# Kernel tuning notes

Hardware: AMD Instinct MI355X
Metric: run time of the kernel (lower is better)

## Reference

```python
import jax, jax.numpy as jnp
import numpy as np

DT = 0.01
NLAG = 50           # int(maxlag / dt), maxlag = 0.5 s
NMA = 20
NC = 8192
NT = 4096


def _xcorr(data1, data2):
    # torch F.conv1d(data1.view(1, nc, nt), data2.view(nc, 1, nt),
    #                padding=NLAG+1, groups=nc)
    # == per-channel sliding cross-correlation.
    lhs = data1[None]            # (1, NC, NT)
    rhs = data2[:, None, :]      # (NC, 1, NT) -- one tiny filter per group
    out = jax.lax.conv_general_dilated(
        lhs, rhs,
        window_strides=(1,),
        padding=[(NLAG + 1, NLAG + 1)],
        dimension_numbers=("NCH", "OIH", "NCH"),
        feature_group_count=NC,
    )
    return out                   # (1, NC, L), L = 2*NLAG + 3 when nt1 == nt2


def _moving_average(x, nma=NMA):
    # Faithful to CCModel.moving_average: AvgPool1d(nma, stride=1, pad=nma//2)
    # applied after permute(0,2,1), i.e. the pooling runs over the CHANNEL
    # axis, with zero padding included in the mean (count_include_pad=True),
    # then sliced back to nc channels.
    nb, nc, L = x.shape
    pad = nma // 2
    xp = jnp.pad(x, ((0, 0), (pad, pad), (0, 0)))
    cs = jnp.concatenate(
        [jnp.zeros((nb, 1, L), x.dtype), jnp.cumsum(xp, axis=1)], axis=1)
    win = (cs[:, nma:, :] - cs[:, :-nma, :]) / nma   # sliding sum / nma
    return win[:, :nc, :]


def _pick_maxabs(R, dt):
    # pick_Rkt_maxabs: per-channel max-|cc| pick.
    L = R.shape[-1]
    nlag_c = (L - 1) // 2        # zero-lag index
    imax = jnp.argmax(jnp.abs(R), axis=-1)                              # (nb, nc)
    vmain = jnp.take_along_axis(R, imax[..., None], axis=-1)[..., 0]    # signed peak
    vpos = jnp.max(R, axis=-1)
    vneg = jnp.min(R, axis=-1)
    vside = jnp.where(vmain >= 0, vneg, vpos)        # opposite-sign extremum
    tmax = (imax - nlag_c).astype(R.dtype) * dt
    return vmain, vside, tmax


def setup_inputs() -> dict:
    key = jax.random.key(0)
    k1, k2, k3, k4 = jax.random.split(key, 4)
    data1 = jax.random.normal(k1, (NC, NT), dtype=jnp.float32)
    data2 = jax.random.normal(k2, (NC, NT), dtype=jnp.float32)
    event1 = jax.random.randint(k3, (1,), 0, 1000, dtype=jnp.int32)
    event2 = jax.random.randint(k4, (1,), 0, 1000, dtype=jnp.int32)
    return {"data1": data1, "data2": data2, "event1": event1, "event2": event2}


def reference(data1, data2, event1, event2):
    xcor = _xcorr(data1, data2)              # (1, NC, 2*NLAG+3)
    xcor = _moving_average(xcor, NMA)        # in-place overwrite in torch
    vmax, vmin, tmax = _pick_maxabs(xcor, DT)
    return xcor, vmax, vmin, tmax
```

## Files before the change

kernel.cpp:

```cpp
#include <hip/hip_runtime.h>

#define NC 8192
#define NT 4096
#define NLAGS 103
#define WS_STRIDE 104
#define LPW 28
#define PADL 51
#define D1LOG 4208
#define PHYS(x) ((x) + (((x) >> 4) << 2))
#define D1P 5260
#define D2P 5120
#define SMEMF (D1P + D2P)
#define XBASE (NC*NLAGS)

__global__ __launch_bounds__(256, 3)
void xcorr_kernel(const float* __restrict__ g1, const float* __restrict__ g2,
                  float* __restrict__ ws) {
    __shared__ __align__(16) float smem[SMEMF];
    float* d1s = smem;
    float* d2s = smem + D1P;
    const int c   = blockIdx.x;
    const int tid = threadIdx.x;
    const float4* r14 = (const float4*)(g1 + (size_t)c * NT);
    const float4* r24 = (const float4*)(g2 + (size_t)c * NT);

    #pragma unroll
    for (int i = 0; i < 4; ++i) {
        float4 v = r14[tid + 256*i];
        int x = PADL + 4*(tid + 256*i);
        d1s[PHYS(x)]   = v.x;
        d1s[PHYS(x+1)] = v.y;
        d1s[PHYS(x+2)] = v.z;
        d1s[PHYS(x+3)] = v.w;
        float4 u = r24[tid + 256*i];
        int y = 4*(tid + 256*i);
        *(float4*)&d2s[PHYS(y)] = u;
    }
    if (tid < PADL) d1s[PHYS(tid)] = 0.f;
    if (tid < 61)   d1s[PHYS(PADL + NT + tid)] = 0.f;
    __syncthreads();

    const int wv   = tid >> 6;
    const int lane = tid & 63;
    const int l0   = wv * LPW;

    float acc[LPW];
    #pragma unroll
    for (int l = 0; l < LPW; ++l) acc[l] = 0.f;

    #pragma unroll 1
    for (int it = 0; it < 4; ++it) {
        const int k0 = it*1024 + lane*16;
        float b[16];
        #pragma unroll
        for (int t = 0; t < 4; ++t) {
            int y = k0 + 4*t;
            float4 v = *(const float4*)&d2s[PHYS(y)];
            b[4*t]=v.x; b[4*t+1]=v.y; b[4*t+2]=v.z; b[4*t+3]=v.w;
        }
        float w[LPW + 16];
        #pragma unroll
        for (int t = 0; t < 11; ++t) {
            int x = k0 + l0 + 4*t;
            float4 v = *(const float4*)&d1s[PHYS(x)];
            w[4*t]=v.x; w[4*t+1]=v.y; w[4*t+2]=v.z; w[4*t+3]=v.w;
        }
        #pragma unroll
        for (int j = 0; j < 16; ++j)
            #pragma unroll
            for (int l = 0; l < LPW; ++l)
                acc[l] = fmaf(w[l+j], b[j], acc[l]);
    }

    __syncthreads();
    float* red = smem + wv * (64*29);
    #pragma unroll
    for (int l = 0; l < LPW; ++l) red[lane*29 + l] = acc[l];
    float sum = 0.f;
    const int lcol = lane & 31;
    const int rb   = lane & 32;
    #pragma unroll
    for (int r = 0; r < 32; ++r) sum += red[(rb + r)*29 + lcol];
    sum += __shfl_down(sum, 32);
    const int L = l0 + lcol;
    if (lane < LPW && L < NLAGS)
        ws[(size_t)c * WS_STRIDE + L] = sum;
}

#define TS 112
__global__ __launch_bounds__(256, 4)
void ma_pick_kernel(const float* __restrict__ ws, float* __restrict__ out) {
    __shared__ float tile[52*TS];
    __shared__ float matile[32*TS];
    const int tid = threadIdx.x;
    const int c0  = blockIdx.x * 32;

    for (int i = tid; i < 52*TS; i += 256) {
        int r   = i / TS;
        int col = i - r*TS;
        int g   = c0 - 10 + r;
        float v = 0.f;
        if (g >= 0 && g < NC && col < NLAGS) v = ws[(size_t)g*WS_STRIDE + col];
        tile[i] = v;
    }
    __syncthreads();

    {
        const int l = tid & 127;
        const int h = tid >> 7;
        if (l < NLAGS) {
            const int cc0 = h * 16;
            float s = 0.f;
            #pragma unroll
            for (int r = 0; r < 20; ++r) s += tile[(cc0 + r)*TS + l];
            #pragma unroll 1
            for (int cc = cc0; cc < cc0 + 16; ++cc) {
                float ma = s / 20.0f;
                matile[cc*TS + l] = ma;
                out[(size_t)(c0 + cc)*NLAGS + l] = ma;
                s += tile[(cc + 20)*TS + l] - tile[cc*TS + l];
            }
        }
    }
    __syncthreads();

    const int wv = tid >> 6, lane = tid & 63;
    #pragma unroll 1
    for (int s8 = 0; s8 < 8; ++s8) {
        const int cc = wv*8 + s8;
        float v1 = matile[cc*TS + lane];
        float a1 = fabsf(v1);
        int   i1 = lane;
        float vmx = v1, vmn = v1;
        if (lane < NLAGS - 64) {
            float v2 = matile[cc*TS + 64 + lane];
            float a2 = fabsf(v2);
            vmx = fmaxf(vmx, v2); vmn = fminf(vmn, v2);
            if (a2 > a1) { a1 = a2; i1 = 64 + lane; v1 = v2; }
        }
        #pragma unroll
        for (int d = 32; d >= 1; d >>= 1) {
            float oa  = __shfl_xor(a1, d);
            int   oi  = __shfl_xor(i1, d);
            float ov  = __shfl_xor(v1, d);
            float omx = __shfl_xor(vmx, d);
            float omn = __shfl_xor(vmn, d);
            vmx = fmaxf(vmx, omx);
            vmn = fminf(vmn, omn);
            if (oa > a1 || (oa == a1 && oi < i1)) { a1 = oa; i1 = oi; v1 = ov; }
        }
        if (lane == 0) {
            const int ch = c0 + cc;
            out[XBASE + ch]        = v1;
            out[XBASE + NC + ch]   = (v1 >= 0.f) ? vmn : vmx;
            out[XBASE + 2*NC + ch] = (float)(i1 - 51) * 0.01f;
        }
    }
}

extern "C" void kernel_launch(void* const* d_in, const int* in_sizes, int n_in,
                              void* d_out, int out_size, void* d_ws, size_t ws_size,
                              hipStream_t stream) {
    const float* g1 = (const float*)d_in[0];
    const float* g2 = (const float*)d_in[1];
    float* out = (float*)d_out;
    float* ws  = (float*)d_ws;

    hipLaunchKernelGGL(xcorr_kernel, dim3(NC), dim3(256), 0, stream, g1, g2, ws);
    hipLaunchKernelGGL(ma_pick_kernel, dim3(NC/32), dim3(256), 0, stream, ws, out);
}
```

Measured before the change: 317.1 us.

## Process four channels per block with double-buffered data1 prefetch

Each xcorr block now handles four channels instead of one and double-buffers the data1 row in shared memory. The next channel's row is prefetched into registers during the current FMA loop, hiding global load latency and cutting block launch overhead. data2 is read straight from global memory into registers with 32 taps per lane rather than being staged in shared memory. This raises register pressure through wider w/b arrays, and the shared-memory reduction now reuses the current buffer.

```diff
diff --git a/kernel.cpp b/kernel.cpp
--- a/kernel.cpp
+++ b/kernel.cpp
@@ -4,87 +4,110 @@
 #define NT 4096
 #define NLAGS 103
 #define WS_STRIDE 104
+#define XBASE (NC*NLAGS)
+
+#define PADL 52
+#define PADR 60
+#define P32(x) ((x) + (((x) >> 5) << 2))
+#define D1PA 4736
+#define SMEMF (2*D1PA)
+#define CPB 4
 #define LPW 28
-#define PADL 51
-#define D1LOG 4208
-#define PHYS(x) ((x) + (((x) >> 4) << 2))
-#define D1P 5260
-#define D2P 5120
-#define SMEMF (D1P + D2P)
-#define XBASE (NC*NLAGS)
+#define REDS 29
 
 __global__ __launch_bounds__(256, 3)
 void xcorr_kernel(const float* __restrict__ g1, const float* __restrict__ g2,
                   float* __restrict__ ws) {
     __shared__ __align__(16) float smem[SMEMF];
-    float* d1s = smem;
-    float* d2s = smem + D1P;
-    const int c   = blockIdx.x;
-    const int tid = threadIdx.x;
-    const float4* r14 = (const float4*)(g1 + (size_t)c * NT);
-    const float4* r24 = (const float4*)(g2 + (size_t)c * NT);
+    const int tid  = threadIdx.x;
+    const int wv   = tid >> 6;
+    const int lane = tid & 63;
+    const int c0   = blockIdx.x * CPB;
 
     #pragma unroll
-    for (int i = 0; i < 4; ++i) {
-        float4 v = r14[tid + 256*i];
-        int x = PADL + 4*(tid + 256*i);
-        d1s[PHYS(x)]   = v.x;
-        d1s[PHYS(x+1)] = v.y;
-        d1s[PHYS(x+2)] = v.z;
-        d1s[PHYS(x+3)] = v.w;
-        float4 u = r24[tid + 256*i];
-        int y = 4*(tid + 256*i);
-        *(float4*)&d2s[PHYS(y)] = u;
+    for (int bb = 0; bb < 2; ++bb) {
+        float* buf = smem + bb * D1PA;
+        if (tid < PADL) buf[P32(tid)] = 0.f;
+        if (tid < PADR) buf[P32(PADL + NT + tid)] = 0.f;
     }
-    if (tid < PADL) d1s[PHYS(tid)] = 0.f;
-    if (tid < 61)   d1s[PHYS(PADL + NT + tid)] = 0.f;
+    {
+        const float4* r = (const float4*)(g1 + (size_t)c0 * NT);
+        #pragma unroll
+        for (int i = 0; i < 4; ++i) {
+            float4 v = r[tid + 256*i];
+            int x = PADL + 4*(tid + 256*i);
+            *(float4*)&smem[P32(x)] = v;
+        }
+    }
     __syncthreads();
 
-    const int wv   = tid >> 6;
-    const int lane = tid & 63;
-    const int l0   = wv * LPW;
+    #pragma unroll 1
+    for (int ci = 0; ci < CPB; ++ci) {
+        const int c = c0 + ci;
+        float* cur  = smem + (ci & 1) * D1PA;
+        float* nxtb = smem + ((ci & 1) ^ 1) * D1PA;
+        const float* g2c = g2 + (size_t)c * NT;
 
-    float acc[LPW];
-    #pragma unroll
-    for (int l = 0; l < LPW; ++l) acc[l] = 0.f;
+        float4 nx0, nx1, nx2, nx3;
+        const bool hasnext = (ci + 1 < CPB);
+        if (hasnext) {
+            const float4* r = (const float4*)(g1 + (size_t)(c + 1) * NT);
+            nx0 = r[tid]; nx1 = r[tid + 256]; nx2 = r[tid + 512]; nx3 = r[tid + 768];
+        }
 
-    #pragma unroll 1
-    for (int it = 0; it < 4; ++it) {
-        const int k0 = it*1024 + lane*16;
-        float b[16];
+        float acc[LPW];
         #pragma unroll
-        for (int t = 0; t < 4; ++t) {
-            int y = k0 + 4*t;
-            float4 v = *(const float4*)&d2s[PHYS(y)];
-            b[4*t]=v.x; b[4*t+1]=v.y; b[4*t+2]=v.z; b[4*t+3]=v.w;
+        for (int l = 0; l < LPW; ++l) acc[l] = 0.f;
+
+        #pragma unroll 1
+        for (int it = 0; it < 2; ++it) {
+            const int k0 = it*2048 + lane*32;
+            float b[32];
+            #pragma unroll
+            for (int t = 0; t < 8; ++t) {
+                float4 v = *(const float4*)(g2c + k0 + 4*t);
+                b[4*t]=v.x; b[4*t+1]=v.y; b[4*t+2]=v.z; b[4*t+3]=v.w;
+            }
+            float w[60];
+            const int wb = k0 + 28*wv;
+            #pragma unroll
+            for (int t = 0; t < 15; ++t) {
+                float4 v = *(const float4*)&cur[P32(wb + 4*t)];
+                w[4*t]=v.x; w[4*t+1]=v.y; w[4*t+2]=v.z; w[4*t+3]=v.w;
+            }
+            #pragma unroll
+            for (int j = 0; j < 32; ++j)
+                #pragma unroll
+                for (int l = 0; l < LPW; ++l)
+                    acc[l] = fmaf(w[l+j], b[j], acc[l]);
         }
-        float w[LPW + 16];
+
+        if (hasnext) {
+            int x = PADL + 4*tid;
+            *(float4*)&nxtb[P32(x)]        = nx0;
+            *(float4*)&nxtb[P32(x + 1024)] = nx1;
+            *(float4*)&nxtb[P32(x + 2048)] = nx2;
+            *(float4*)&nxtb[P32(x + 3072)] = nx3;
+        }
+        __syncthreads();
+
         #pragma unroll
-        for (int t = 0; t < 11; ++t) {
-            int x = k0 + l0 + 4*t;
-            float4 v = *(const float4*)&d1s[PHYS(x)];
-            w[4*t]=v.x; w[4*t+1]=v.y; w[4*t+2]=v.z; w[4*t+3]=v.w;
+        for (int l = 0; l < LPW; ++l) acc[l] += __shfl_down(acc[l], 32);
+        float* red = cur + wv * (32*REDS);
+        if (lane < 32) {
+            #pragma unroll
+            for (int l = 0; l < LPW; ++l) red[lane*REDS + l] = acc[l];
         }
-        #pragma unroll
-        for (int j = 0; j < 16; ++j)
+        if (lane < LPW) {
+            float sum = 0.f;
             #pragma unroll
-            for (int l = 0; l < LPW; ++l)
-                acc[l] = fmaf(w[l+j], b[j], acc[l]);
+            for (int r = 0; r < 32; ++r) sum += red[r*REDS + lane];
+            const int L = 28*wv - 1 + lane;
+            if (L >= 0 && L < NLAGS) ws[(size_t)c * WS_STRIDE + L] = sum;
+        }
+        if (tid < PADL) cur[P32(tid)] = 0.f;
+        __syncthreads();
     }
-
-    __syncthreads();
-    float* red = smem + wv * (64*29);
-    #pragma unroll
-    for (int l = 0; l < LPW; ++l) red[lane*29 + l] = acc[l];
-    float sum = 0.f;
-    const int lcol = lane & 31;
-    const int rb   = lane & 32;
-    #pragma unroll
-    for (int r = 0; r < 32; ++r) sum += red[(rb + r)*29 + lcol];
-    sum += __shfl_down(sum, 32);
-    const int L = l0 + lcol;
-    if (lane < LPW && L < NLAGS)
-        ws[(size_t)c * WS_STRIDE + L] = sum;
 }
 
 #define TS 112
@@ -166,6 +189,6 @@
     float* out = (float*)d_out;
     float* ws  = (float*)d_ws;
 
-    hipLaunchKernelGGL(xcorr_kernel, dim3(NC), dim3(256), 0, stream, g1, g2, ws);
+    hipLaunchKernelGGL(xcorr_kernel, dim3(NC/CPB), dim3(256), 0, stream, g1, g2, ws);
     hipLaunchKernelGGL(ma_pick_kernel, dim3(NC/32), dim3(256), 0, stream, ws, out);
 }
```

Measured after the change: 324.5 us. +2.3%, slower.
